# Kernel tuning notes

Hardware: AMD Instinct MI355X
Metric: run time of the kernel (lower is better)

Reference implementation:

```python
import jax, jax.numpy as jnp
import numpy as np

SCALE = 16.0 / 8.0  # alpha / rank


def setup_inputs() -> dict:
    key = jax.random.key(0)
    ks = jax.random.split(key, 5)
    d_in, d_out, rank = 4096, 4096, 8
    x = jax.random.normal(ks[0], (4, 2048, d_in), dtype=jnp.float32)
    base_weight = jax.random.normal(ks[1], (d_out, d_in), dtype=jnp.float32) * 0.02
    lora_A = jax.random.normal(ks[2], (rank, d_in), dtype=jnp.float32) * 0.02
    lora_B = jax.random.normal(ks[3], (d_out, rank), dtype=jnp.float32) * 0.02
    bias = jax.random.normal(ks[4], (d_out,), dtype=jnp.float32) * 0.02
    return {"x": x, "base_weight": base_weight, "lora_A": lora_A,
            "lora_B": lora_B, "bias": bias}


def reference(x, base_weight, lora_A, lora_B, bias):
    # weight = base + scale * (B @ A)   -> [d_out, d_in]
    weight = base_weight + SCALE * (lora_B @ lora_A)
    # F.linear: x @ weight.T + bias
    return jnp.einsum('bsi,oi->bso', x, weight) + bias
```

## Files before the change

### kernel.cpp

```cpp
#include <hip/hip_runtime.h>
#include <hip/hip_bf16.h>
#include <cstdio>


using bf16   = __bf16;
using bf16x4 = __attribute__((ext_vector_type(4))) __bf16;
using bf16x8 = __attribute__((ext_vector_type(8))) __bf16;
using f32x4  = __attribute__((ext_vector_type(4))) float;

#define TM 128
#define TN 128
#define BK 64

__global__ __launch_bounds__(256) void prep_x(const float* __restrict__ x,
                                              bf16* __restrict__ Xb, long n8) {
    const long stride = (long)gridDim.x * blockDim.x;
    for (long i = (long)blockIdx.x * blockDim.x + threadIdx.x; i < n8; i += stride) {
        const float4 a = reinterpret_cast<const float4*>(x)[2 * i];
        const float4 b = reinterpret_cast<const float4*>(x)[2 * i + 1];
        bf16x8 o;
        o[0] = (bf16)a.x; o[1] = (bf16)a.y; o[2] = (bf16)a.z; o[3] = (bf16)a.w;
        o[4] = (bf16)b.x; o[5] = (bf16)b.y; o[6] = (bf16)b.z; o[7] = (bf16)b.w;
        reinterpret_cast<bf16x8*>(Xb)[i] = o;
    }
}

__global__ __launch_bounds__(256) void prep_w(const float* __restrict__ base,
                                              const float* __restrict__ A,
                                              const float* __restrict__ Bm,
                                              bf16* __restrict__ Wb,
                                              int K, int rank, float scale) {
    const int o = blockIdx.x;
    float br[8];
    const int rr = rank < 8 ? rank : 8;
    for (int r = 0; r < rr; ++r) br[r] = scale * Bm[(size_t)o * rank + r];

    const float* brow = base + (size_t)o * K;
    bf16*        wrow = Wb + (size_t)o * K;

    for (int c = threadIdx.x * 8; c < K; c += 256 * 8) {
        float4 s0 = *reinterpret_cast<const float4*>(brow + c);
        float4 s1 = *reinterpret_cast<const float4*>(brow + c + 4);
        if (rank == 8) {
#pragma unroll
            for (int r = 0; r < 8; ++r) {
                const float4 a0 = *reinterpret_cast<const float4*>(A + (size_t)r * K + c);
                const float4 a1 = *reinterpret_cast<const float4*>(A + (size_t)r * K + c + 4);
                s0.x += br[r] * a0.x; s0.y += br[r] * a0.y;
                s0.z += br[r] * a0.z; s0.w += br[r] * a0.w;
                s1.x += br[r] * a1.x; s1.y += br[r] * a1.y;
                s1.z += br[r] * a1.z; s1.w += br[r] * a1.w;
            }
        } else {
            for (int r = 0; r < rank; ++r) {
                const float b = scale * Bm[(size_t)o * rank + r];
                const float4 a0 = *reinterpret_cast<const float4*>(A + (size_t)r * K + c);
                const float4 a1 = *reinterpret_cast<const float4*>(A + (size_t)r * K + c + 4);
                s0.x += b * a0.x; s0.y += b * a0.y; s0.z += b * a0.z; s0.w += b * a0.w;
                s1.x += b * a1.x; s1.y += b * a1.y; s1.z += b * a1.z; s1.w += b * a1.w;
            }
        }
        bf16x8 ov;
        ov[0] = (bf16)s0.x; ov[1] = (bf16)s0.y; ov[2] = (bf16)s0.z; ov[3] = (bf16)s0.w;
        ov[4] = (bf16)s1.x; ov[5] = (bf16)s1.y; ov[6] = (bf16)s1.z; ov[7] = (bf16)s1.w;
        *reinterpret_cast<bf16x8*>(wrow + c) = ov;
    }
}

__global__ __launch_bounds__(256) void gemm_bt_bf16(
    const bf16* __restrict__ Xb,
    const bf16* __restrict__ Wb,
    const float* __restrict__ bias,
    float* __restrict__ out,
    int M, int N, int K)
{
    __shared__ __align__(16) bf16 As[TM * BK];
    __shared__ __align__(16) bf16 Bs[TN * BK];

    const int tid  = threadIdx.x;
    const int lane = tid & 63;
    const int wv   = tid >> 6;
    const int wm   = wv >> 1;
    const int wn   = wv & 1;
    const int m0   = blockIdx.y * TM;
    const int n0   = blockIdx.x * TN;

    const int r16 = lane & 15;
    const int q   = lane >> 4;
    const int xv  = r16 & 7;

    const int srow = lane >> 3;
    const int scol = ((lane & 7) ^ (srow & 7)) * 8;

    const bf16* gA[4];
    const bf16* gB[4];
#pragma unroll
    for (int i = 0; i < 4; ++i) {
        const int grp = i * 4 + wv;
        const int row = grp * 8 + srow;
        gA[i] = Xb + (size_t)(m0 + row) * K + scol;
        gB[i] = Wb + (size_t)(n0 + row) * K + scol;
    }

    int ao[2][4], bo[2][4];
#pragma unroll
    for (int ks = 0; ks < 2; ++ks) {
        const int off = ((ks * 4 + q) ^ xv) * 8;
#pragma unroll
        for (int t = 0; t < 4; ++t) {
            ao[ks][t] = (wm * 64 + t * 16 + r16) * BK + off;
            bo[ks][t] = (wn * 64 + t * 16 + r16) * BK + off;
        }
    }

    f32x4 acc[4][4] = {};

    for (int k0 = 0; k0 < K; k0 += BK) {
#pragma unroll
        for (int i = 0; i < 4; ++i) {
            const int grp = i * 4 + wv;
            __builtin_amdgcn_global_load_lds(
                (const __attribute__((address_space(1))) void*)gA[i],
                (__attribute__((address_space(3))) void*)(As + grp * 512),
                16, 0, 0);
            __builtin_amdgcn_global_load_lds(
                (const __attribute__((address_space(1))) void*)gB[i],
                (__attribute__((address_space(3))) void*)(Bs + grp * 512),
                16, 0, 0);
            gA[i] += BK;
            gB[i] += BK;
        }
        __syncthreads();

#pragma unroll
        for (int ks = 0; ks < 2; ++ks) {
            bf16x8 afrag[4], bfrag[4];
#pragma unroll
            for (int t = 0; t < 4; ++t) {
                afrag[t] = *reinterpret_cast<const bf16x8*>(&As[ao[ks][t]]);
                bfrag[t] = *reinterpret_cast<const bf16x8*>(&Bs[bo[ks][t]]);
            }
#pragma unroll
            for (int mi = 0; mi < 4; ++mi)
#pragma unroll
                for (int ni = 0; ni < 4; ++ni)
                    acc[mi][ni] = __builtin_amdgcn_mfma_f32_16x16x32_bf16(
                        afrag[mi], bfrag[ni], acc[mi][ni], 0, 0, 0);
        }
        __syncthreads();
    }

#pragma unroll
    for (int mi = 0; mi < 4; ++mi) {
#pragma unroll
        for (int ni = 0; ni < 4; ++ni) {
            const int gr = m0 + wm * 64 + mi * 16 + q * 4;
            const int gc = n0 + wn * 64 + ni * 16 + r16;
            const float bv = bias[gc];
#pragma unroll
            for (int r = 0; r < 4; ++r)
                out[(size_t)(gr + r) * N + gc] = acc[mi][ni][r] + bv;
        }
    }
}

extern "C" void kernel_launch(void* const* d_in, const int* in_sizes, int n_in,
                              void* d_out, int out_size, void* d_ws, size_t ws_size,
                              hipStream_t stream) {
    const float* x    = (const float*)d_in[0];
    const float* base = (const float*)d_in[1];
    const float* lA   = (const float*)d_in[2];
    const float* lB   = (const float*)d_in[3];
    const float* bias = (const float*)d_in[4];
    float* out = (float*)d_out;

    const int  N    = in_sizes[4];
    const int  rank = in_sizes[3] / N;
    const int  K    = in_sizes[2] / rank;
    const long M    = (long)in_sizes[0] / K;
    const float scale = 16.0f / (float)rank;

    bf16* Xb = (bf16*)d_ws;
    bf16* Wb = Xb + (size_t)M * K;
    const size_t need = ((size_t)M * K + (size_t)N * K) * sizeof(bf16);
    if (ws_size < need) {
        fprintf(stderr, "kernel_launch: ws_size %zu < needed %zu\n", ws_size, need);
        return;
    }

    const long n8x = (long)M * K / 8;
    long blk = (n8x + 255) / 256;
    if (blk > 2048) blk = 2048;
    prep_x<<<dim3((unsigned)blk), dim3(256), 0, stream>>>(x, Xb, n8x);

    prep_w<<<dim3((unsigned)N), dim3(256), 0, stream>>>(base, lA, lB, Wb, K, rank, scale);

    gemm_bt_bf16<<<dim3(N / TN, (unsigned)(M / TM)), dim3(256), 0, stream>>>(
        Xb, Wb, bias, out, (int)M, N, K);
}
```

Baseline: 584.9 us.

## Rewrite GEMM as 256x256 double-buffered, 8-wave phased pipeline with prefetch

Replaces the 128x128 single-buffered GEMM with a 256x256 tile kernel using 512 threads (8 waves), double-buffered LDS split into two K-halves, and a four-phase schedule. Each phase issues the next tile's global-to-LDS loads while MFMAs run, using explicit vmcnt waits, barriers, and setprio. The goal is to hide global load latency, remove the serialized load-sync-compute pattern, and raise data reuse per tile. It uses more LDS and registers (128 accumulator floats per thread), and the grid is smaller, which may reduce occupancy and tail balance.

Measured after the change: 542.9 us. -7.2%, faster.

```diff
diff --git a/kernel.cpp b/kernel.cpp
--- a/kernel.cpp
+++ b/kernel.cpp
@@ -4,12 +4,11 @@
 
 
 using bf16   = __bf16;
-using bf16x4 = __attribute__((ext_vector_type(4))) __bf16;
 using bf16x8 = __attribute__((ext_vector_type(8))) __bf16;
 using f32x4  = __attribute__((ext_vector_type(4))) float;
 
-#define TM 128
-#define TN 128
+#define BM 256
+#define BN 256
 #define BK 64
 
 __global__ __launch_bounds__(256) void prep_x(const float* __restrict__ x,
@@ -67,101 +66,184 @@
     }
 }
 
-__global__ __launch_bounds__(256) void gemm_bt_bf16(
+__global__ __launch_bounds__(512, 2) void gemm_8ph(
     const bf16* __restrict__ Xb,
     const bf16* __restrict__ Wb,
     const float* __restrict__ bias,
     float* __restrict__ out,
     int M, int N, int K)
 {
-    __shared__ __align__(16) bf16 As[TM * BK];
-    __shared__ __align__(16) bf16 Bs[TN * BK];
+    __shared__ __align__(16) bf16 As[2 * 2 * 256 * 32];
+    __shared__ __align__(16) bf16 Bs[2 * 2 * 256 * 32];
 
     const int tid  = threadIdx.x;
     const int lane = tid & 63;
     const int wv   = tid >> 6;
-    const int wm   = wv >> 1;
-    const int wn   = wv & 1;
-    const int m0   = blockIdx.y * TM;
-    const int n0   = blockIdx.x * TN;
+    const int wm   = wv >> 2;
+    const int wn   = wv & 3;
+    const int m0   = blockIdx.y * BM;
+    const int n0   = blockIdx.x * BN;
 
     const int r16 = lane & 15;
     const int q   = lane >> 4;
-    const int xv  = r16 & 7;
-
-    const int srow = lane >> 3;
-    const int scol = ((lane & 7) ^ (srow & 7)) * 8;
-
-    const bf16* gA[4];
-    const bf16* gB[4];
-#pragma unroll
-    for (int i = 0; i < 4; ++i) {
-        const int grp = i * 4 + wv;
-        const int row = grp * 8 + srow;
-        gA[i] = Xb + (size_t)(m0 + row) * K + scol;
-        gB[i] = Wb + (size_t)(n0 + row) * K + scol;
-    }
-
-    int ao[2][4], bo[2][4];
-#pragma unroll
-    for (int ks = 0; ks < 2; ++ks) {
-        const int off = ((ks * 4 + q) ^ xv) * 8;
-#pragma unroll
-        for (int t = 0; t < 4; ++t) {
-            ao[ks][t] = (wm * 64 + t * 16 + r16) * BK + off;
-            bo[ks][t] = (wn * 64 + t * 16 + r16) * BK + off;
-        }
-    }
-
-    f32x4 acc[4][4] = {};
-
-    for (int k0 = 0; k0 < K; k0 += BK) {
-#pragma unroll
-        for (int i = 0; i < 4; ++i) {
-            const int grp = i * 4 + wv;
-            __builtin_amdgcn_global_load_lds(
-                (const __attribute__((address_space(1))) void*)gA[i],
-                (__attribute__((address_space(3))) void*)(As + grp * 512),
-                16, 0, 0);
-            __builtin_amdgcn_global_load_lds(
-                (const __attribute__((address_space(1))) void*)gB[i],
-                (__attribute__((address_space(3))) void*)(Bs + grp * 512),
-                16, 0, 0);
-            gA[i] += BK;
-            gB[i] += BK;
-        }
-        __syncthreads();
-
-#pragma unroll
-        for (int ks = 0; ks < 2; ++ks) {
-            bf16x8 afrag[4], bfrag[4];
-#pragma unroll
-            for (int t = 0; t < 4; ++t) {
-                afrag[t] = *reinterpret_cast<const bf16x8*>(&As[ao[ks][t]]);
-                bfrag[t] = *reinterpret_cast<const bf16x8*>(&Bs[bo[ks][t]]);
-            }
-#pragma unroll
-            for (int mi = 0; mi < 4; ++mi)
-#pragma unroll
-                for (int ni = 0; ni < 4; ++ni)
-                    acc[mi][ni] = __builtin_amdgcn_mfma_f32_16x16x32_bf16(
-                        afrag[mi], bfrag[ni], acc[mi][ni], 0, 0, 0);
-        }
-        __syncthreads();
-    }
-
-#pragma unroll
-    for (int mi = 0; mi < 4; ++mi) {
-#pragma unroll
-        for (int ni = 0; ni < 4; ++ni) {
-            const int gr = m0 + wm * 64 + mi * 16 + q * 4;
-            const int gc = n0 + wn * 64 + ni * 16 + r16;
+    const int cq  = (q ^ ((r16 >> 1) & 3)) * 8;
+
+    const bf16* srcA[2];
+    const bf16* srcB[2];
+#pragma unroll
+    for (int i = 0; i < 2; ++i) {
+        const int slot = i * 512 + tid;
+        const int row  = slot >> 2;
+        const int c    = (tid & 3) ^ ((row >> 1) & 3);
+        srcA[i] = Xb + (size_t)(m0 + row) * K + c * 8;
+        srcB[i] = Wb + (size_t)(n0 + row) * K + c * 8;
+    }
+    const int dst0 = (0 * 512 + wv * 64) * 8;
+    const int dst1 = (1 * 512 + wv * 64) * 8;
+
+#define STAGE_A(buf, kh, koff)                                                        \
+    do {                                                                              \
+        __builtin_amdgcn_global_load_lds(                                             \
+            (const __attribute__((address_space(1))) void*)(srcA[0] + (koff) + (kh) * 32), \
+            (__attribute__((address_space(3))) void*)(As + (buf) * 16384 + (kh) * 8192 + dst0), \
+            16, 0, 0);                                                                \
+        __builtin_amdgcn_global_load_lds(                                             \
+            (const __attribute__((address_space(1))) void*)(srcA[1] + (koff) + (kh) * 32), \
+            (__attribute__((address_space(3))) void*)(As + (buf) * 16384 + (kh) * 8192 + dst1), \
+            16, 0, 0);                                                                \
+    } while (0)
+#define STAGE_B(buf, kh, koff)                                                        \
+    do {                                                                              \
+        __builtin_amdgcn_global_load_lds(                                             \
+            (const __attribute__((address_space(1))) void*)(srcB[0] + (koff) + (kh) * 32), \
+            (__attribute__((address_space(3))) void*)(Bs + (buf) * 16384 + (kh) * 8192 + dst0), \
+            16, 0, 0);                                                                \
+        __builtin_amdgcn_global_load_lds(                                             \
+            (const __attribute__((address_space(1))) void*)(srcB[1] + (koff) + (kh) * 32), \
+            (__attribute__((address_space(3))) void*)(Bs + (buf) * 16384 + (kh) * 8192 + dst1), \
+            16, 0, 0);                                                                \
+    } while (0)
+
+    int aoff[2][4], boff[4];
+#pragma unroll
+    for (int mh = 0; mh < 2; ++mh)
+#pragma unroll
+        for (int f = 0; f < 4; ++f)
+            aoff[mh][f] = (wm * 128 + mh * 64 + f * 16 + r16) * 32 + cq;
+#pragma unroll
+    for (int f = 0; f < 4; ++f)
+        boff[f] = (wn * 64 + f * 16 + r16) * 32 + cq;
+
+    f32x4 acc[8][4] = {};
+
+    STAGE_A(0, 0, 0);
+    STAGE_B(0, 0, 0);
+    STAGE_A(0, 1, 0);
+    STAGE_B(0, 1, 0);
+    asm volatile("s_waitcnt vmcnt(4)" ::: "memory");
+    __builtin_amdgcn_s_barrier();
+
+    const int NT = K / BK;
+    for (int t = 0; t < NT; ++t) {
+        const int cur  = t & 1;
+        const int nxt  = cur ^ 1;
+        const int koff = (t + 1) * BK;
+        const bool pre = (t + 1 < NT);
+        bf16x8 bf[4], af[4];
+
+        {
+            const bf16* Ab = As + cur * 16384;
+            const bf16* Bb = Bs + cur * 16384;
+#pragma unroll
+            for (int f = 0; f < 4; ++f) bf[f] = *reinterpret_cast<const bf16x8*>(Bb + boff[f]);
+#pragma unroll
+            for (int f = 0; f < 4; ++f) af[f] = *reinterpret_cast<const bf16x8*>(Ab + aoff[0][f]);
+            if (pre) STAGE_A(nxt, 0, koff);
+            __builtin_amdgcn_s_barrier();
+            asm volatile("s_waitcnt lgkmcnt(0)" ::: "memory");
+            __builtin_amdgcn_sched_barrier(0);
+            __builtin_amdgcn_s_setprio(1);
+#pragma unroll
+            for (int f = 0; f < 4; ++f)
+#pragma unroll
+                for (int n = 0; n < 4; ++n)
+                    acc[f][n] = __builtin_amdgcn_mfma_f32_16x16x32_bf16(af[f], bf[n], acc[f][n], 0, 0, 0);
+            __builtin_amdgcn_s_setprio(0);
+            __builtin_amdgcn_s_barrier();
+        }
+        {
+            const bf16* Ab = As + cur * 16384;
+#pragma unroll
+            for (int f = 0; f < 4; ++f) af[f] = *reinterpret_cast<const bf16x8*>(Ab + aoff[1][f]);
+            if (pre) STAGE_B(nxt, 0, koff);
+            if (t == NT - 1) asm volatile("s_waitcnt vmcnt(0)" ::: "memory");
+            else             asm volatile("s_waitcnt vmcnt(4)" ::: "memory");
+            __builtin_amdgcn_s_barrier();
+            asm volatile("s_waitcnt lgkmcnt(0)" ::: "memory");
+            __builtin_amdgcn_sched_barrier(0);
+            __builtin_amdgcn_s_setprio(1);
+#pragma unroll
+            for (int f = 0; f < 4; ++f)
+#pragma unroll
+                for (int n = 0; n < 4; ++n)
+                    acc[4 + f][n] = __builtin_amdgcn_mfma_f32_16x16x32_bf16(af[f], bf[n], acc[4 + f][n], 0, 0, 0);
+            __builtin_amdgcn_s_setprio(0);
+            __builtin_amdgcn_s_barrier();
+        }
+        {
+            const bf16* Ab = As + cur * 16384 + 8192;
+            const bf16* Bb = Bs + cur * 16384 + 8192;
+#pragma unroll
+            for (int f = 0; f < 4; ++f) bf[f] = *reinterpret_cast<const bf16x8*>(Bb + boff[f]);
+#pragma unroll
+            for (int f = 0; f < 4; ++f) af[f] = *reinterpret_cast<const bf16x8*>(Ab + aoff[0][f]);
+            if (pre) STAGE_A(nxt, 1, koff);
+            __builtin_amdgcn_s_barrier();
+            asm volatile("s_waitcnt lgkmcnt(0)" ::: "memory");
+            __builtin_amdgcn_sched_barrier(0);
+            __builtin_amdgcn_s_setprio(1);
+#pragma unroll
+            for (int f = 0; f < 4; ++f)
+#pragma unroll
+                for (int n = 0; n < 4; ++n)
+                    acc[f][n] = __builtin_amdgcn_mfma_f32_16x16x32_bf16(af[f], bf[n], acc[f][n], 0, 0, 0);
+            __builtin_amdgcn_s_setprio(0);
+            __builtin_amdgcn_s_barrier();
+        }
+        {
+            const bf16* Ab = As + cur * 16384 + 8192;
+#pragma unroll
+            for (int f = 0; f < 4; ++f) af[f] = *reinterpret_cast<const bf16x8*>(Ab + aoff[1][f]);
+            if (pre) STAGE_B(nxt, 1, koff);
+            asm volatile("s_waitcnt vmcnt(4)" ::: "memory");
+            __builtin_amdgcn_s_barrier();
+            asm volatile("s_waitcnt lgkmcnt(0)" ::: "memory");
+            __builtin_amdgcn_sched_barrier(0);
+            __builtin_amdgcn_s_setprio(1);
+#pragma unroll
+            for (int f = 0; f < 4; ++f)
+#pragma unroll
+                for (int n = 0; n < 4; ++n)
+                    acc[4 + f][n] = __builtin_amdgcn_mfma_f32_16x16x32_bf16(af[f], bf[n], acc[4 + f][n], 0, 0, 0);
+            __builtin_amdgcn_s_setprio(0);
+            __builtin_amdgcn_s_barrier();
+        }
+    }
+
+#pragma unroll
+    for (int mf = 0; mf < 8; ++mf) {
+        const int gr = m0 + wm * 128 + (mf >> 2) * 64 + (mf & 3) * 16 + q * 4;
+#pragma unroll
+        for (int nf = 0; nf < 4; ++nf) {
+            const int gc = n0 + wn * 64 + nf * 16 + r16;
             const float bv = bias[gc];
 #pragma unroll
             for (int r = 0; r < 4; ++r)
-                out[(size_t)(gr + r) * N + gc] = acc[mi][ni][r] + bv;
-        }
-    }
+                out[(size_t)(gr + r) * N + gc] = acc[mf][nf][r] + bv;
+        }
+    }
+#undef STAGE_A
+#undef STAGE_B
 }
 
 extern "C" void kernel_launch(void* const* d_in, const int* in_sizes, int n_in,
@@ -195,6 +277,6 @@
 
     prep_w<<<dim3((unsigned)N), dim3(256), 0, stream>>>(base, lA, lB, Wb, K, rank, scale);
 
-    gemm_bt_bf16<<<dim3(N / TN, (unsigned)(M / TM)), dim3(256), 0, stream>>>(
+    gemm_8ph<<<dim3(N / BN, (unsigned)(M / BM)), dim3(512), 0, stream>>>(
         Xb, Wb, bias, out, (int)M, N, K);
 }
```
